# Performance work log

Measured on AMD Instinct MI355X. Metric: run time of the kernel, lower is better.

## Reference

```python
import jax, jax.numpy as jnp
import numpy as np

UNITS = 512
EPS = 1e-6

def setup_inputs() -> dict:
    key = jax.random.key(0)
    x = jax.random.normal(key, (262144, UNITS), dtype=jnp.float32)
    return {"x": x}

def reference(x):
    d = x.shape[1]
    # Gram matrix with diagonal jitter: [d, d]
    g = x.T @ x + jnp.eye(d, dtype=x.dtype) * EPS
    L = jnp.linalg.cholesky(g)  # lower triangular [d, d]
    # inv(L) via triangular solve (same math as tf.linalg.inv on L)
    L_inv = jax.scipy.linalg.solve_triangular(L, jnp.eye(d, dtype=x.dtype), lower=True)
    ortho_weights = L_inv.T * jnp.sqrt(jnp.float32(UNITS))
    return x @ ortho_weights
```

## Files before the change

### kernel.cpp

```cpp
#include <hip/hip_runtime.h>


#define EPSJ 1e-6f
#define SQRTD 22.627416997969522f

typedef short bf16x8 __attribute__((ext_vector_type(8)));
typedef float f32x4 __attribute__((ext_vector_type(4)));

__device__ __forceinline__ unsigned short f2bf(float f) {
  unsigned u = __float_as_uint(f);
  unsigned r = u + 0x7fffu + ((u >> 16) & 1u);
  return (unsigned short)(r >> 16);
}

__device__ __forceinline__ int swz(int row, int slot) {
  return slot ^ ((row ^ (row >> 3)) & 7);
}

__device__ __forceinline__ float wred(float s) {
  s += __shfl_xor(s, 1);  s += __shfl_xor(s, 2);  s += __shfl_xor(s, 4);
  s += __shfl_xor(s, 8);  s += __shfl_xor(s, 16); s += __shfl_xor(s, 32);
  return s;
}

#define GLOAD16(g, l)                                                         \
  __builtin_amdgcn_global_load_lds(                                           \
      (const __attribute__((address_space(1))) void*)(g),                     \
      (__attribute__((address_space(3))) void*)(l), 16, 0, 0)

__global__ void convert_bf(const float* __restrict__ X,
                           unsigned short* __restrict__ Xbf) {
  long idx = (long)blockIdx.x * blockDim.x + threadIdx.x;
  const long stride = (long)gridDim.x * blockDim.x;
  const long nch = 134217728 / 8;
  for (long i = idx; i < nch; i += stride) {
    float4 f0 = ((const float4*)X)[i * 2];
    float4 f1 = ((const float4*)X)[i * 2 + 1];
    uint4 o;
    o.x = (unsigned)f2bf(f0.x) | ((unsigned)f2bf(f0.y) << 16);
    o.y = (unsigned)f2bf(f0.z) | ((unsigned)f2bf(f0.w) << 16);
    o.z = (unsigned)f2bf(f1.x) | ((unsigned)f2bf(f1.y) << 16);
    o.w = (unsigned)f2bf(f1.z) | ((unsigned)f2bf(f1.w) << 16);
    ((uint4*)Xbf)[i] = o;
  }
}

__device__ __forceinline__ void stage_pack(const unsigned short* __restrict__ src,
                                           unsigned short* dst, int c0, int k) {
  uint4 a = *(const uint4*)src;
  uint4 b = *(const uint4*)(src + 512);
  unsigned av[4] = {a.x, a.y, a.z, a.w}, bv[4] = {b.x, b.y, b.z, b.w};
  int k7 = (k & 7) * 2, khi = k >> 3;
  #pragma unroll
  for (int j = 0; j < 4; ++j) {
    int cA = c0 + 2 * j, cB = cA + 1;
    unsigned lo = (av[j] & 0xFFFFu) | (bv[j] << 16);
    unsigned hi = (av[j] >> 16) | (bv[j] & 0xFFFF0000u);
    int slA = khi ^ ((cA ^ (cA >> 3)) & 7);
    int slB = khi ^ ((cB ^ (cB >> 3)) & 7);
    *(unsigned*)((char*)dst + cA * 128 + slA * 16 + k7) = lo;
    *(unsigned*)((char*)dst + cB * 128 + slB * 16 + k7) = hi;
  }
}

__global__ __launch_bounds__(512, 2) void gram_bf(
    const unsigned short* __restrict__ Xbf, float* __restrict__ part,
    int nchunk) {
  __shared__ unsigned short As[256 * 64];
  __shared__ unsigned short Bs[256 * 64];
  const int b = blockIdx.x, pos = b % 3, chunk = b / 3;
  const int s0 = (int)((long)4096 * chunk / nchunk);
  const int s1 = (int)((long)4096 * (chunk + 1) / nchunk);
  const int ca = (pos == 1) ? 256 : 0;
  const int cb2 = (pos == 0) ? 0 : 256;
  const bool diag = (pos != 2);
  const int t = threadIdx.x, lane = t & 63, w = t >> 6;
  const int wr = w >> 2, wc = w & 3;

  f32x4 acc[8][4];
  const f32x4 zf = {0.f, 0.f, 0.f, 0.f};
  #pragma unroll
  for (int a = 0; a < 8; ++a)
    #pragma unroll
    for (int bb = 0; bb < 4; ++bb) acc[a][bb] = zf;

  const int c0 = (t & 31) * 8;
  const int kp = t >> 5;

  for (int ks = s0; ks < s1; ++ks) {
    long rb = (long)ks * 64;
    #pragma unroll
    for (int it = 0; it < 2; ++it) {
      int k = it * 32 + kp * 2;
      long r = rb + k;
      stage_pack(Xbf + r * 512 + ca + c0, As, c0, k);
      if (!diag) stage_pack(Xbf + r * 512 + cb2 + c0, Bs, c0, k);
    }
    __syncthreads();
    const unsigned short* Bp = diag ? As : Bs;
    #pragma unroll
    for (int kk = 0; kk < 2; ++kk) {
      bf16x8 af[8], bfr[4];
      #pragma unroll
      for (int fm = 0; fm < 8; ++fm) {
        int row = wr * 128 + fm * 16 + (lane & 15);
        int slot = swz(row, kk * 4 + (lane >> 4));
        af[fm] = *(const bf16x8*)((const char*)As + row * 128 + slot * 16);
      }
      #pragma unroll
      for (int fn = 0; fn < 4; ++fn) {
        int row = wc * 64 + fn * 16 + (lane & 15);
        int slot = swz(row, kk * 4 + (lane >> 4));
        bfr[fn] = *(const bf16x8*)((const char*)Bp + row * 128 + slot * 16);
      }
      #pragma unroll
      for (int fm = 0; fm < 8; ++fm)
        #pragma unroll
        for (int fn = 0; fn < 4; ++fn)
          acc[fm][fn] = __builtin_amdgcn_mfma_f32_16x16x32_bf16(
              af[fm], bfr[fn], acc[fm][fn], 0, 0, 0);
    }
    __syncthreads();
  }
  float* out = part + (long)b * 65536;
  #pragma unroll
  for (int fm = 0; fm < 8; ++fm)
    #pragma unroll
    for (int fn = 0; fn < 4; ++fn)
      #pragma unroll
      for (int j = 0; j < 4; ++j) {
        int i  = wr * 128 + fm * 16 + (lane >> 4) * 4 + j;
        int jj = wc * 64 + fn * 16 + (lane & 15);
        out[i * 256 + jj] = acc[fm][fn][j];
      }
}

__global__ __launch_bounds__(512, 2) void gram_f32(
    const float* __restrict__ X, float* __restrict__ part, int nchunk) {
  __shared__ unsigned short As[256 * 64];
  __shared__ unsigned short Bs[256 * 64];
  const int b = blockIdx.x;
  const int pos = b % 3;
  const int chunk = b / 3;
  const int CR = 262144 / nchunk;
  const long r0 = (long)chunk * CR;
  const int ca = (pos == 1) ? 256 : 0;
  const int cb = (pos == 0) ? 0 : 256;
  const bool diag = (pos != 2);
  const int t = threadIdx.x, lane = t & 63, w = t >> 6;
  const int wr = w >> 2, wc = w & 3;

  f32x4 acc[8][4];
  const f32x4 zf = {0.f, 0.f, 0.f, 0.f};
  #pragma unroll
  for (int a = 0; a < 8; ++a)
    #pragma unroll
    for (int bb = 0; bb < 4; ++bb) acc[a][bb] = zf;

  const int c_oct = t & 31, msub = t >> 5;

  for (int ks = 0; ks < CR; ks += 64) {
    #pragma unroll
    for (int it = 0; it < 4; ++it) {
      int m = msub + 16 * it;
      long row = r0 + ks + m;
      const float4* sa = (const float4*)(X + row * 512 + ca + c_oct * 8);
      float4 a0 = sa[0], a1 = sa[1];
      {
        float v[8] = {a0.x, a0.y, a0.z, a0.w, a1.x, a1.y, a1.z, a1.w};
        #pragma unroll
        for (int s = 0; s < 8; ++s) {
          int c = c_oct * 8 + s;
          int off = c * 128 + ((2 * m) ^ (((c ^ (c >> 3)) & 7) << 4));
          *(unsigned short*)((char*)As + off) = f2bf(v[s]);
        }
      }
      if (!diag) {
        const float4* sb = (const float4*)(X + row * 512 + cb + c_oct * 8);
        float4 b0 = sb[0], b1 = sb[1];
        float v[8] = {b0.x, b0.y, b0.z, b0.w, b1.x, b1.y, b1.z, b1.w};
        #pragma unroll
        for (int s = 0; s < 8; ++s) {
          int c = c_oct * 8 + s;
          int off = c * 128 + ((2 * m) ^ (((c ^ (c >> 3)) & 7) << 4));
          *(unsigned short*)((char*)Bs + off) = f2bf(v[s]);
        }
      }
    }
    __syncthreads();
    const unsigned short* Bp = diag ? As : Bs;
    #pragma unroll
    for (int kk = 0; kk < 2; ++kk) {
      bf16x8 af[8], bfr[4];
      #pragma unroll
      for (int fm = 0; fm < 8; ++fm) {
        int row = wr * 128 + fm * 16 + (lane & 15);
        int slot = swz(row, kk * 4 + (lane >> 4));
        af[fm] = *(const bf16x8*)((const char*)As + row * 128 + slot * 16);
      }
      #pragma unroll
      for (int fn = 0; fn < 4; ++fn) {
        int row = wc * 64 + fn * 16 + (lane & 15);
        int slot = swz(row, kk * 4 + (lane >> 4));
        bfr[fn] = *(const bf16x8*)((const char*)Bp + row * 128 + slot * 16);
      }
      #pragma unroll
      for (int fm = 0; fm < 8; ++fm)
        #pragma unroll
        for (int fn = 0; fn < 4; ++fn)
          acc[fm][fn] = __builtin_amdgcn_mfma_f32_16x16x32_bf16(
              af[fm], bfr[fn], acc[fm][fn], 0, 0, 0);
    }
    __syncthreads();
  }
  float* out = part + (long)b * 65536;
  #pragma unroll
  for (int fm = 0; fm < 8; ++fm)
    #pragma unroll
    for (int fn = 0; fn < 4; ++fn)
      #pragma unroll
      for (int j = 0; j < 4; ++j) {
        int i  = wr * 128 + fm * 16 + (lane >> 4) * 4 + j;
        int jj = wc * 64 + fn * 16 + (lane & 15);
        out[i * 256 + jj] = acc[fm][fn][j];
      }
}

__global__ void gram_reduce(const float* __restrict__ part,
                            float* __restrict__ G, int nchunk) {
  int idx = blockIdx.x * 256 + threadIdx.x;
  int pos = idx >> 16;
  int e = idx & 65535;
  float s = 0.f;
  for (int ch = 0; ch < nchunk; ++ch)
    s += part[(long)(ch * 3 + pos) * 65536 + e];
  int i = e >> 8, j = e & 255;
  if (pos == 0) {
    G[i * 512 + j] = s;
  } else if (pos == 1) {
    G[(256 + i) * 512 + 256 + j] = s;
  } else {
    G[i * 512 + 256 + j] = s;
    G[(256 + j) * 512 + i] = s;
  }
}

__global__ void chol_diag(float* __restrict__ G, int c0) {
  __shared__ float P[128][129];
  int t = threadIdx.x;
  for (int idx = t; idx < 128 * 128; idx += 512) {
    int i = idx >> 7, j = idx & 127;
    float v = G[(long)(c0 + i) * 512 + c0 + j];
    if (i == j) v += EPSJ;
    P[i][j] = v;
  }
  __syncthreads();
  int lane = t & 63, w = t >> 6;
  for (int sp = 0; sp < 4; ++sp) {
    int b0 = sp * 32;
    if (w == 0) {
      float r[32];
      #pragma unroll
      for (int k = 0; k < 32; ++k) r[k] = (lane < 32) ? P[b0 + lane][b0 + k] : 0.f;
      #pragma unroll
      for (int j = 0; j < 32; ++j) {
        float d = sqrtf(__shfl(r[j], j));
        if (lane == j) r[j] = d;
        else if (lane > j && lane < 32) r[j] = r[j] / d;
        float rj = r[j];
        #pragma unroll
        for (int k = j + 1; k < 32; ++k) {
          float Lkj = __shfl(rj, k);
          if (lane > j && lane < 32) r[k] -= rj * Lkj;
        }
      }
      #pragma unroll
      for (int k = 0; k < 32; ++k) if (lane < 32) P[b0 + lane][b0 + k] = r[k];
    }
    __syncthreads();
    int nb = 128 - (b0 + 32);
    if (nb > 0) {
      if (t < nb) {
        int rr = b0 + 32 + t;
        float x[32];
        #pragma unroll
        for (int j = 0; j < 32; ++j) x[j] = P[rr][b0 + j];
        #pragma unroll
        for (int j = 0; j < 32; ++j) {
          float xj = x[j] / P[b0 + j][b0 + j];
          x[j] = xj;
          #pragma unroll
          for (int k2 = j + 1; k2 < 32; ++k2) x[k2] -= xj * P[b0 + k2][b0 + j];
        }
        #pragma unroll
        for (int j = 0; j < 32; ++j) P[rr][b0 + j] = x[j];
      }
      __syncthreads();
      int total = nb * nb;
      for (int idx = t; idx < total; idx += 512) {
        int i = b0 + 32 + idx / nb, k = b0 + 32 + idx % nb;
        float s = P[i][k];
        #pragma unroll
        for (int j = 0; j < 32; ++j) s -= P[i][b0 + j] * P[k][b0 + j];
        P[i][k] = s;
      }
      __syncthreads();
    }
  }
  for (int idx = t; idx < 128 * 128; idx += 512) {
    int i = idx >> 7, j = idx & 127;
    G[(long)(c0 + i) * 512 + c0 + j] = P[i][j];
  }
}

__global__ void chol_solve(float* __restrict__ G, int p) {
  int c0 = 128 * p;
  int row0 = c0 + 128;
  int w = threadIdx.x >> 6, lane = threadIdx.x & 63;
  long r = row0 + blockIdx.x * 4 + w;
  float x[2];
  x[0] = G[r * 512 + c0 + lane];
  x[1] = G[r * 512 + c0 + 64 + lane];
  #pragma unroll
  for (int q = 0; q < 2; ++q) {
    for (int ii = 0; ii < 64; ++ii) {
      int i = q * 64 + ii;
      const float* Lrow = G + (long)(c0 + i) * 512 + c0;
      float s = 0.f;
      if (q == 1) s += x[0] * Lrow[lane];
      s += (lane < ii) ? x[q] * Lrow[q * 64 + lane] : 0.f;
      s = wred(s);
      float ai = __shfl(x[q], ii);
      float xi = (ai - s) / Lrow[i];
      if (lane == ii) x[q] = xi;
    }
  }
  G[r * 512 + c0 + lane] = x[0];
  G[r * 512 + c0 + 64 + lane] = x[1];
}

__global__ void chol_syrk(float* __restrict__ G, int t0) {
  int id = blockIdx.x;
  int ti = 0;
  while ((ti + 1) * (ti + 2) / 2 <= id) ++ti;
  int tj = id - ti * (ti + 1) / 2;
  __shared__ float As2[64][130], Bs2[64][130];
  int t = threadIdx.x;
  int c0 = t0 - 128;
  for (int idx = t; idx < 64 * 128; idx += 256) {
    int i = idx >> 7, j = idx & 127;
    As2[i][j] = G[(long)(t0 + 64 * ti + i) * 512 + c0 + j];
    Bs2[i][j] = G[(long)(t0 + 64 * tj + i) * 512 + c0 + j];
  }
  __syncthreads();
  int tr = (t >> 4) * 4, tc = (t & 15) * 4;
  float cacc[4][4];
  #pragma unroll
  for (int u = 0; u < 4; ++u)
    #pragma unroll
    for (int v = 0; v < 4; ++v) cacc[u][v] = 0.f;
  for (int k = 0; k < 128; ++k) {
    float a4[4], b4[4];
    #pragma unroll
    for (int u = 0; u < 4; ++u) { a4[u] = As2[tr + u][k]; b4[u] = Bs2[tc + u][k]; }
    #pragma unroll
    for (int u = 0; u < 4; ++u)
      #pragma unroll
      for (int v = 0; v < 4; ++v) cacc[u][v] += a4[u] * b4[v];
  }
  #pragma unroll
  for (int u = 0; u < 4; ++u)
    #pragma unroll
    for (int v = 0; v < 4; ++v)
      G[(long)(t0 + 64 * ti + tr + u) * 512 + t0 + 64 * tj + tc + v] -= cacc[u][v];
}

template <bool SWZ>
__global__ void tri_inv(const float* __restrict__ G,
                        unsigned short* __restrict__ Wt) {
  int w = threadIdx.x >> 6, lane = threadIdx.x & 63;
  int c = blockIdx.x * 4 + w;
  float v8[8];
  #pragma unroll
  for (int q = 0; q < 8; ++q) v8[q] = 0.f;
  #pragma unroll
  for (int q = 0; q < 8; ++q) {
    for (int ii = 0; ii < 64; ++ii) {
      int i = q * 64 + ii;
      const float* Lrow = G + (long)i * 512;
      float s = 0.f;
      #pragma unroll
      for (int qq = 0; qq < 8; ++qq) {
        if (qq < q) s += v8[qq] * Lrow[qq * 64 + lane];
      }
      s += (lane < ii) ? v8[q] * Lrow[q * 64 + lane] : 0.f;
      s = wred(s);
      float xi = (((i == c) ? 1.f : 0.f) - s) / Lrow[i];
      if (lane == ii) v8[q] = xi;
    }
  }
  if (SWZ) {
    int ko = (c >> 3) & 7, jj = c & 7, cb = c & ~63;
    #pragma unroll
    for (int q = 0; q < 8; ++q) {
      int n = q * 64 + lane;
      int sl = ko ^ ((n ^ (n >> 3)) & 7);
      Wt[(long)n * 512 + cb + sl * 8 + jj] = f2bf(SQRTD * v8[q]);
    }
  } else {
    #pragma unroll
    for (int q = 0; q < 8; ++q) {
      int i = q * 64 + lane;
      Wt[(long)i * 512 + c] = f2bf(SQRTD * v8[q]);
    }
  }
}

__global__ __launch_bounds__(256, 2) void ymm2(
    const unsigned short* __restrict__ Xbf,
    const unsigned short* __restrict__ Wt, float* __restrict__ Y) {
  __shared__ unsigned short As[2][128 * 64];
  __shared__ unsigned short Bs[2][128 * 64];
  const int t = threadIdx.x, lane = t & 63, w = t >> 6;
  const long m0 = (long)blockIdx.y * 128;
  const int n0 = blockIdx.x * 128;
  const int wm = (w >> 1) * 64, wn = (w & 1) * 64;
  const int lrow = lane >> 3, lslot = lane & 7;
  f32x4 acc[4][4];
  const f32x4 zf = {0.f, 0.f, 0.f, 0.f};
  #pragma unroll
  for (int a = 0; a < 4; ++a)
    #pragma unroll
    for (int bq = 0; bq < 4; ++bq) acc[a][bq] = zf;

  auto stage = [&](int buf, int k0) {
    #pragma unroll
    for (int j = 0; j < 4; ++j) {
      int row = (w * 4 + j) * 8 + lrow;
      const unsigned short* sA =
          Xbf + (m0 + row) * 512 + k0 + swz(row, lslot) * 8;
      const unsigned short* sB =
          Wt + (long)(n0 + row) * 512 + k0 + lslot * 8;
      GLOAD16(sA, &As[buf][(w * 4 + j) * 512]);
      GLOAD16(sB, &Bs[buf][(w * 4 + j) * 512]);
    }
  };
  auto compute = [&](int buf) {
    #pragma unroll
    for (int kk = 0; kk < 2; ++kk) {
      bf16x8 af[4], bfr[4];
      #pragma unroll
      for (int fm = 0; fm < 4; ++fm) {
        int row = wm + fm * 16 + (lane & 15);
        af[fm] = *(const bf16x8*)((const char*)As[buf] + row * 128 +
                                  swz(row, kk * 4 + (lane >> 4)) * 16);
      }
      #pragma unroll
      for (int fn = 0; fn < 4; ++fn) {
        int row = wn + fn * 16 + (lane & 15);
        bfr[fn] = *(const bf16x8*)((const char*)Bs[buf] + row * 128 +
                                   swz(row, kk * 4 + (lane >> 4)) * 16);
      }
      #pragma unroll
      for (int fm = 0; fm < 4; ++fm)
        #pragma unroll
        for (int fn = 0; fn < 4; ++fn)
          acc[fm][fn] = __builtin_amdgcn_mfma_f32_16x16x32_bf16(
              af[fm], bfr[fn], acc[fm][fn], 0, 0, 0);
    }
  };

  stage(0, 0);
  __syncthreads();
  int cur = 0;
  #pragma unroll 1
  for (int kt = 0; kt < 7; ++kt) {
    stage(cur ^ 1, (kt + 1) * 64);
    compute(cur);
    __syncthreads();
    cur ^= 1;
  }
  compute(cur);

  #pragma unroll
  for (int fm = 0; fm < 4; ++fm)
    #pragma unroll
    for (int fn = 0; fn < 4; ++fn)
      #pragma unroll
      for (int j = 0; j < 4; ++j) {
        long row = m0 + wm + fm * 16 + (lane >> 4) * 4 + j;
        int col = n0 + wn + fn * 16 + (lane & 15);
        Y[row * 512 + col] = acc[fm][fn][j];
      }
}

__global__ __launch_bounds__(256) void ymm_v1(const float* __restrict__ X,
                                              const unsigned short* __restrict__ Wt,
                                              float* __restrict__ Y) {
  __shared__ unsigned short As[128 * 64];
  __shared__ unsigned short Bs[128 * 64];
  const int t = threadIdx.x, lane = t & 63, w = t >> 6;
  const long m0 = (long)blockIdx.x * 128;
  const int n0 = blockIdx.y * 128;
  const int wm = (w >> 1) * 64, wn = (w & 1) * 64;
  f32x4 acc[4][4];
  const f32x4 zf = {0.f, 0.f, 0.f, 0.f};
  #pragma unroll
  for (int a = 0; a < 4; ++a)
    #pragma unroll
    for (int bq = 0; bq < 4; ++bq) acc[a][bq] = zf;
  const int ko = t & 7, mrow = t >> 3;

  for (int k0 = 0; k0 < 512; k0 += 64) {
    #pragma unroll
    for (int it = 0; it < 4; ++it) {
      int m = mrow + 32 * it;
      const float4* src = (const float4*)(X + (m0 + m) * 512 + k0 + ko * 8);
      float4 f0 = src[0], f1 = src[1];
      unsigned p0 = (unsigned)f2bf(f0.x) | ((unsigned)f2bf(f0.y) << 16);
      unsigned p1 = (unsigned)f2bf(f0.z) | ((unsigned)f2bf(f0.w) << 16);
      unsigned p2 = (unsigned)f2bf(f1.x) | ((unsigned)f2bf(f1.y) << 16);
      unsigned p3 = (unsigned)f2bf(f1.z) | ((unsigned)f2bf(f1.w) << 16);
      int slot = swz(m, ko);
      *(uint4*)((char*)As + m * 128 + slot * 16) = make_uint4(p0, p1, p2, p3);
    }
    #pragma unroll
    for (int it = 0; it < 4; ++it) {
      int n = mrow + 32 * it;
      uint4 raw = *(const uint4*)(Wt + (long)(n0 + n) * 512 + k0 + ko * 8);
      int slot = swz(n, ko);
      *(uint4*)((char*)Bs + n * 128 + slot * 16) = raw;
    }
    __syncthreads();
    #pragma unroll
    for (int kk = 0; kk < 2; ++kk) {
      bf16x8 af[4], bfr[4];
      #pragma unroll
      for (int fm = 0; fm < 4; ++fm) {
        int row = wm + fm * 16 + (lane & 15);
        af[fm] = *(const bf16x8*)((const char*)As + row * 128 +
                                  swz(row, kk * 4 + (lane >> 4)) * 16);
      }
      #pragma unroll
      for (int fn = 0; fn < 4; ++fn) {
        int row = wn + fn * 16 + (lane & 15);
        bfr[fn] = *(const bf16x8*)((const char*)Bs + row * 128 +
                                   swz(row, kk * 4 + (lane >> 4)) * 16);
      }
      #pragma unroll
      for (int fm = 0; fm < 4; ++fm)
        #pragma unroll
        for (int fn = 0; fn < 4; ++fn)
          acc[fm][fn] = __builtin_amdgcn_mfma_f32_16x16x32_bf16(
              af[fm], bfr[fn], acc[fm][fn], 0, 0, 0);
    }
    __syncthreads();
  }
  #pragma unroll
  for (int fm = 0; fm < 4; ++fm)
    #pragma unroll
    for (int fn = 0; fn < 4; ++fn)
      #pragma unroll
      for (int j = 0; j < 4; ++j) {
        long row = m0 + wm + fm * 16 + (lane >> 4) * 4 + j;
        int col = n0 + wn + fn * 16 + (lane & 15);
        Y[row * 512 + col] = acc[fm][fn][j];
      }
}

static void chol_chain(float* G, hipStream_t stream) {
  for (int p = 0; p < 4; ++p) {
    chol_diag<<<1, 512, 0, stream>>>(G, 128 * p);
    if (p < 3) {
      int row0 = 128 * (p + 1);
      chol_solve<<<(512 - row0) / 4, 256, 0, stream>>>(G, p);
      int nt = (512 - row0) / 64;
      chol_syrk<<<nt * (nt + 1) / 2, 256, 0, stream>>>(G, row0);
    }
  }
}

extern "C" void kernel_launch(void* const* d_in, const int* in_sizes, int n_in,
                              void* d_out, int out_size, void* d_ws, size_t ws_size,
                              hipStream_t stream) {
  const float* X = (const float*)d_in[0];
  float* Y = (float*)d_out;
  char* ws = (char*)d_ws;
  float* G = (float*)ws;
  unsigned short* Wt = (unsigned short*)(ws + (1 << 20));
  char* wsp = ws + (1 << 20) + (1 << 19);

  const int NCH_FAST = 85;
  size_t part_bytes = (size_t)NCH_FAST * 3 * 65536 * 4;
  size_t xbf_off = (size_t)(1 << 20) + (1 << 19) + part_bytes;
  size_t need = xbf_off + (size_t)134217728 * 2;

  if (ws_size >= need) {
    float* part = (float*)wsp;
    unsigned short* Xbf = (unsigned short*)(ws + xbf_off);
    convert_bf<<<2048, 256, 0, stream>>>(X, Xbf);
    gram_bf<<<3 * NCH_FAST, 512, 0, stream>>>(Xbf, part, NCH_FAST);
    gram_reduce<<<768, 256, 0, stream>>>(part, G, NCH_FAST);
    chol_chain(G, stream);
    tri_inv<true><<<128, 256, 0, stream>>>(G, Wt);
    ymm2<<<dim3(4, 2048), 256, 0, stream>>>(Xbf, Wt, Y);
  } else {
    float* part = (float*)wsp;
    size_t fixed = (size_t)(1 << 20) + (1 << 19);
    int nchunk = 64;
    while (nchunk > 1 && fixed + (size_t)nchunk * 3 * 65536 * 4 > ws_size)
      nchunk >>= 1;
    gram_f32<<<3 * nchunk, 512, 0, stream>>>(X, part, nchunk);
    gram_reduce<<<768, 256, 0, stream>>>(part, G, nchunk);
    chol_chain(G, stream);
    tri_inv<false><<<128, 256, 0, stream>>>(G, Wt);
    ymm_v1<<<dim3(2048, 4), 256, 0, stream>>>(X, Wt, Y);
  }
}
```

Before: 1.464 ms.

## Blocked triangular inverse, 64-wide Cholesky panels, and vectorized MFMA output stores

Replaces the per-column serial triangular inverse with a blocked scheme: each 64x64 diagonal block is inverted by its own kernel, and the off-diagonal blocks are assembled with small register-tiled GEMMs. The diagonal Cholesky kernel now uses 64-wide panels with a register-tiled trailing update. The MFMA operands are swapped so each lane holds four contiguous output columns, allowing float4 stores in the gram and Y GEMMs. The goal is to cut the long serial latency of the small-matrix stages and the cost of scattered scalar stores, at the price of more kernels and more complex code.

```diff
diff --git a/kernel.cpp b/kernel.cpp
--- a/kernel.cpp
+++ b/kernel.cpp
@@ -118,7 +118,7 @@
         #pragma unroll
         for (int fn = 0; fn < 4; ++fn)
           acc[fm][fn] = __builtin_amdgcn_mfma_f32_16x16x32_bf16(
-              af[fm], bfr[fn], acc[fm][fn], 0, 0, 0);
+              bfr[fn], af[fm], acc[fm][fn], 0, 0, 0);
     }
     __syncthreads();
   }
@@ -126,13 +126,11 @@
   #pragma unroll
   for (int fm = 0; fm < 8; ++fm)
     #pragma unroll
-    for (int fn = 0; fn < 4; ++fn)
-      #pragma unroll
-      for (int j = 0; j < 4; ++j) {
-        int i  = wr * 128 + fm * 16 + (lane >> 4) * 4 + j;
-        int jj = wc * 64 + fn * 16 + (lane & 15);
-        out[i * 256 + jj] = acc[fm][fn][j];
-      }
+    for (int fn = 0; fn < 4; ++fn) {
+      int mi = wr * 128 + fm * 16 + (lane & 15);
+      int nj = wc * 64 + fn * 16 + (lane >> 4) * 4;
+      *(float4*)(out + mi * 256 + nj) = *(float4*)&acc[fm][fn];
+    }
 }
 
 __global__ __launch_bounds__(512, 2) void gram_f32(
@@ -245,7 +243,7 @@
   }
 }
 
-__global__ void chol_diag(float* __restrict__ G, int c0) {
+__global__ __launch_bounds__(512) void chol_diag(float* __restrict__ G, int c0) {
   __shared__ float P[128][129];
   int t = threadIdx.x;
   for (int idx = t; idx < 128 * 128; idx += 512) {
@@ -256,57 +254,67 @@
   }
   __syncthreads();
   int lane = t & 63, w = t >> 6;
-  for (int sp = 0; sp < 4; ++sp) {
-    int b0 = sp * 32;
+  #pragma unroll
+  for (int sp = 0; sp < 2; ++sp) {
+    int b0 = sp * 64;
     if (w == 0) {
-      float r[32];
-      #pragma unroll
-      for (int k = 0; k < 32; ++k) r[k] = (lane < 32) ? P[b0 + lane][b0 + k] : 0.f;
-      #pragma unroll
-      for (int j = 0; j < 32; ++j) {
+      float r[64];
+      #pragma unroll
+      for (int k = 0; k < 64; ++k) r[k] = P[b0 + lane][b0 + k];
+      #pragma unroll
+      for (int j = 0; j < 64; ++j) {
         float d = sqrtf(__shfl(r[j], j));
         if (lane == j) r[j] = d;
-        else if (lane > j && lane < 32) r[j] = r[j] / d;
+        else if (lane > j) r[j] = r[j] / d;
         float rj = r[j];
         #pragma unroll
-        for (int k = j + 1; k < 32; ++k) {
+        for (int k = j + 1; k < 64; ++k) {
           float Lkj = __shfl(rj, k);
-          if (lane > j && lane < 32) r[k] -= rj * Lkj;
+          if (lane > j) r[k] -= rj * Lkj;
         }
       }
       #pragma unroll
-      for (int k = 0; k < 32; ++k) if (lane < 32) P[b0 + lane][b0 + k] = r[k];
-    }
-    __syncthreads();
-    int nb = 128 - (b0 + 32);
-    if (nb > 0) {
-      if (t < nb) {
-        int rr = b0 + 32 + t;
-        float x[32];
-        #pragma unroll
-        for (int j = 0; j < 32; ++j) x[j] = P[rr][b0 + j];
-        #pragma unroll
-        for (int j = 0; j < 32; ++j) {
-          float xj = x[j] / P[b0 + j][b0 + j];
+      for (int k = 0; k < 64; ++k) P[b0 + lane][b0 + k] = r[k];
+    }
+    __syncthreads();
+    if (sp == 0) {
+      if (t < 64) {
+        int rr = 64 + t;
+        float x[64];
+        #pragma unroll
+        for (int j = 0; j < 64; ++j) x[j] = P[rr][j];
+        #pragma unroll
+        for (int j = 0; j < 64; ++j) {
+          float xj = x[j] / P[j][j];
           x[j] = xj;
           #pragma unroll
-          for (int k2 = j + 1; k2 < 32; ++k2) x[k2] -= xj * P[b0 + k2][b0 + j];
+          for (int k2 = j + 1; k2 < 64; ++k2) x[k2] -= xj * P[k2][j];
         }
         #pragma unroll
-        for (int j = 0; j < 32; ++j) P[rr][b0 + j] = x[j];
+        for (int j = 0; j < 64; ++j) P[rr][j] = x[j];
       }
       __syncthreads();
-      int total = nb * nb;
-      for (int idx = t; idx < total; idx += 512) {
-        int i = b0 + 32 + idx / nb, k = b0 + 32 + idx % nb;
-        float s = P[i][k];
-        #pragma unroll
-        for (int j = 0; j < 32; ++j) s -= P[i][b0 + j] * P[k][b0 + j];
-        P[i][k] = s;
+      int or_ = (t >> 5) * 4;
+      int oc = (t & 31) * 2;
+      float cc[4][2] = {{0,0},{0,0},{0,0},{0,0}};
+      for (int k = 0; k < 64; ++k) {
+        float a0 = P[64 + or_][k],     a1 = P[64 + or_ + 1][k];
+        float a2 = P[64 + or_ + 2][k], a3 = P[64 + or_ + 3][k];
+        float e0 = P[64 + oc][k],      e1 = P[64 + oc + 1][k];
+        cc[0][0] += a0 * e0; cc[0][1] += a0 * e1;
+        cc[1][0] += a1 * e0; cc[1][1] += a1 * e1;
+        cc[2][0] += a2 * e0; cc[2][1] += a2 * e1;
+        cc[3][0] += a3 * e0; cc[3][1] += a3 * e1;
+      }
+      #pragma unroll
+      for (int u = 0; u < 4; ++u) {
+        P[64 + or_ + u][64 + oc]     -= cc[u][0];
+        P[64 + or_ + u][64 + oc + 1] -= cc[u][1];
       }
       __syncthreads();
     }
   }
+  __syncthreads();
   for (int idx = t; idx < 128 * 128; idx += 512) {
     int i = idx >> 7, j = idx & 127;
     G[(long)(c0 + i) * 512 + c0 + j] = P[i][j];
@@ -375,7 +383,104 @@
       G[(long)(t0 + 64 * ti + tr + u) * 512 + t0 + 64 * tj + tc + v] -= cacc[u][v];
 }
 
-template <bool SWZ>
+__global__ __launch_bounds__(64) void dinv64(const float* __restrict__ G,
+                                             float* __restrict__ Dinv) {
+  __shared__ float Lb[64][65];
+  int p = blockIdx.x;
+  int lane = threadIdx.x;
+  for (int i = 0; i < 64; ++i)
+    Lb[i][lane] = (lane <= i) ? G[(long)(64 * p + i) * 512 + 64 * p + lane] : 0.f;
+  __syncthreads();
+  float x[64];
+  #pragma unroll
+  for (int i = 0; i < 64; ++i) {
+    float s = (i == lane) ? 1.f : 0.f;
+    #pragma unroll
+    for (int j = 0; j < i; ++j) s -= Lb[i][j] * x[j];
+    x[i] = s / Lb[i][i];
+  }
+  #pragma unroll
+  for (int i = 0; i < 64; ++i)
+    Dinv[p * 4096 + i * 64 + lane] = x[i];
+}
+
+__global__ __launch_bounds__(256) void tri_assemble(
+    const float* __restrict__ G, const float* __restrict__ Dinv,
+    unsigned short* __restrict__ Wt) {
+  __shared__ float Bsh[448 * 64];
+  __shared__ float T[64 * 64];
+  const int q = blockIdx.x, t = threadIdx.x;
+  const int or_ = (t >> 4) * 4, oc = (t & 15) * 4;
+
+  for (int p = q + 1; p < 8; ++p) {
+    float cc[4][4] = {{0}};
+    for (int r = q; r < p; ++r) {
+      const float* Lbase = G + (long)(64 * p) * 512 + 64 * r;
+      #pragma unroll 4
+      for (int k = 0; k < 64; ++k) {
+        float a0 = Lbase[(or_ + 0) * 512 + k];
+        float a1 = Lbase[(or_ + 1) * 512 + k];
+        float a2 = Lbase[(or_ + 2) * 512 + k];
+        float a3 = Lbase[(or_ + 3) * 512 + k];
+        float b0, b1, b2, b3;
+        if (r == q) {
+          const float* Bq = Dinv + q * 4096 + k * 64 + oc;
+          b0 = Bq[0]; b1 = Bq[1]; b2 = Bq[2]; b3 = Bq[3];
+        } else {
+          const float* Br = Bsh + ((r - q - 1) * 64 + k) * 64 + oc;
+          b0 = Br[0]; b1 = Br[1]; b2 = Br[2]; b3 = Br[3];
+        }
+        cc[0][0] += a0*b0; cc[0][1] += a0*b1; cc[0][2] += a0*b2; cc[0][3] += a0*b3;
+        cc[1][0] += a1*b0; cc[1][1] += a1*b1; cc[1][2] += a1*b2; cc[1][3] += a1*b3;
+        cc[2][0] += a2*b0; cc[2][1] += a2*b1; cc[2][2] += a2*b2; cc[2][3] += a2*b3;
+        cc[3][0] += a3*b0; cc[3][1] += a3*b1; cc[3][2] += a3*b2; cc[3][3] += a3*b3;
+      }
+    }
+    #pragma unroll
+    for (int u = 0; u < 4; ++u)
+      #pragma unroll
+      for (int v = 0; v < 4; ++v)
+        T[(or_ + u) * 64 + oc + v] = cc[u][v];
+    __syncthreads();
+
+    float c2[4][4] = {{0}};
+    const float* Dp = Dinv + p * 4096;
+    #pragma unroll 4
+    for (int k = 0; k < 64; ++k) {
+      float a0 = Dp[(or_ + 0) * 64 + k];
+      float a1 = Dp[(or_ + 1) * 64 + k];
+      float a2 = Dp[(or_ + 2) * 64 + k];
+      float a3 = Dp[(or_ + 3) * 64 + k];
+      const float* Tk = T + k * 64 + oc;
+      float b0 = Tk[0], b1 = Tk[1], b2 = Tk[2], b3 = Tk[3];
+      c2[0][0] += a0*b0; c2[0][1] += a0*b1; c2[0][2] += a0*b2; c2[0][3] += a0*b3;
+      c2[1][0] += a1*b0; c2[1][1] += a1*b1; c2[1][2] += a1*b2; c2[1][3] += a1*b3;
+      c2[2][0] += a2*b0; c2[2][1] += a2*b1; c2[2][2] += a2*b2; c2[2][3] += a2*b3;
+      c2[3][0] += a3*b0; c2[3][1] += a3*b1; c2[3][2] += a3*b2; c2[3][3] += a3*b3;
+    }
+    #pragma unroll
+    for (int u = 0; u < 4; ++u)
+      #pragma unroll
+      for (int v = 0; v < 4; ++v)
+        Bsh[((p - q - 1) * 64 + or_ + u) * 64 + oc + v] = -c2[u][v];
+    __syncthreads();
+  }
+
+  const int nr = (8 - q) * 64;
+  for (int idx = t; idx < nr * 64; idx += 256) {
+    int i = idx >> 6, kk = idx & 63;
+    float v = (i < 64) ? Dinv[q * 4096 + i * 64 + kk]
+                       : Bsh[(i - 64) * 64 + kk];
+    int n = 64 * q + i;
+    int sl = (kk >> 3) ^ ((n ^ (n >> 3)) & 7);
+    Wt[(long)n * 512 + 64 * q + sl * 8 + (kk & 7)] = f2bf(SQRTD * v);
+  }
+  for (int idx = t; idx < 64 * q * 64; idx += 256) {
+    int n = idx >> 6, kk = idx & 63;
+    Wt[(long)n * 512 + 64 * q + kk] = 0;
+  }
+}
+
 __global__ void tri_inv(const float* __restrict__ G,
                         unsigned short* __restrict__ Wt) {
   int w = threadIdx.x >> 6, lane = threadIdx.x & 63;
@@ -399,20 +504,10 @@
       if (lane == ii) v8[q] = xi;
     }
   }
-  if (SWZ) {
-    int ko = (c >> 3) & 7, jj = c & 7, cb = c & ~63;
-    #pragma unroll
-    for (int q = 0; q < 8; ++q) {
-      int n = q * 64 + lane;
-      int sl = ko ^ ((n ^ (n >> 3)) & 7);
-      Wt[(long)n * 512 + cb + sl * 8 + jj] = f2bf(SQRTD * v8[q]);
-    }
-  } else {
-    #pragma unroll
-    for (int q = 0; q < 8; ++q) {
-      int i = q * 64 + lane;
-      Wt[(long)i * 512 + c] = f2bf(SQRTD * v8[q]);
-    }
+  #pragma unroll
+  for (int q = 0; q < 8; ++q) {
+    int i = q * 64 + lane;
+    Wt[(long)i * 512 + c] = f2bf(SQRTD * v8[q]);
   }
 }
 
@@ -466,7 +561,7 @@
         #pragma unroll
         for (int fn = 0; fn < 4; ++fn)
           acc[fm][fn] = __builtin_amdgcn_mfma_f32_16x16x32_bf16(
-              af[fm], bfr[fn], acc[fm][fn], 0, 0, 0);
+              bfr[fn], af[fm], acc[fm][fn], 0, 0, 0);
     }
   };
 
@@ -485,13 +580,11 @@
   #pragma unroll
   for (int fm = 0; fm < 4; ++fm)
     #pragma unroll
-    for (int fn = 0; fn < 4; ++fn)
-      #pragma unroll
-      for (int j = 0; j < 4; ++j) {
-        long row = m0 + wm + fm * 16 + (lane >> 4) * 4 + j;
-        int col = n0 + wn + fn * 16 + (lane & 15);
-        Y[row * 512 + col] = acc[fm][fn][j];
-      }
+    for (int fn = 0; fn < 4; ++fn) {
+      long row = m0 + wm + fm * 16 + (lane & 15);
+      int col = n0 + wn + fn * 16 + (lane >> 4) * 4;
+      *(float4*)(Y + row * 512 + col) = *(float4*)&acc[fm][fn];
+    }
 }
 
 __global__ __launch_bounds__(256) void ymm_v1(const float* __restrict__ X,
@@ -588,24 +681,26 @@
   char* ws = (char*)d_ws;
   float* G = (float*)ws;
   unsigned short* Wt = (unsigned short*)(ws + (1 << 20));
-  char* wsp = ws + (1 << 20) + (1 << 19);
+  float* Dinv = (float*)(ws + (1 << 20) + (1 << 19));
 
   const int NCH_FAST = 85;
+  size_t part_off = (size_t)(2 << 20);
   size_t part_bytes = (size_t)NCH_FAST * 3 * 65536 * 4;
-  size_t xbf_off = (size_t)(1 << 20) + (1 << 19) + part_bytes;
+  size_t xbf_off = part_off + part_bytes;
   size_t need = xbf_off + (size_t)134217728 * 2;
 
   if (ws_size >= need) {
-    float* part = (float*)wsp;
+    float* part = (float*)(ws + part_off);
     unsigned short* Xbf = (unsigned short*)(ws + xbf_off);
     convert_bf<<<2048, 256, 0, stream>>>(X, Xbf);
     gram_bf<<<3 * NCH_FAST, 512, 0, stream>>>(Xbf, part, NCH_FAST);
     gram_reduce<<<768, 256, 0, stream>>>(part, G, NCH_FAST);
     chol_chain(G, stream);
-    tri_inv<true><<<128, 256, 0, stream>>>(G, Wt);
+    dinv64<<<8, 64, 0, stream>>>(G, Dinv);
+    tri_assemble<<<8, 256, 0, stream>>>(G, Dinv, Wt);
     ymm2<<<dim3(4, 2048), 256, 0, stream>>>(Xbf, Wt, Y);
   } else {
-    float* part = (float*)wsp;
+    float* part = (float*)(ws + (1 << 20) + (1 << 19));
     size_t fixed = (size_t)(1 << 20) + (1 << 19);
     int nchunk = 64;
     while (nchunk > 1 && fixed + (size_t)nchunk * 3 * 65536 * 4 > ws_size)
@@ -613,7 +708,7 @@
     gram_f32<<<3 * nchunk, 512, 0, stream>>>(X, part, nchunk);
     gram_reduce<<<768, 256, 0, stream>>>(part, G, nchunk);
     chol_chain(G, stream);
-    tri_inv<false><<<128, 256, 0, stream>>>(G, Wt);
+    tri_inv<<<128, 256, 0, stream>>>(G, Wt);
     ymm_v1<<<dim3(2048, 4), 256, 0, stream>>>(X, Wt, Y);
   }
 }
```

New measurement: 2.202 ms. 50.4% more time.
